# Optimization experiments

Hardware: AMD Instinct MI355X
Metric: run time of the kernel (lower is better)

The kernel has to match this reference:

```python
import jax, jax.numpy as jnp
import numpy as np

N_NODES = 87381  # complete 4-ary tree of depth 9: (4**9 - 1) / 3
VOCAB = 32000
D_IN = 256
M_DIM = 256


def setup_inputs() -> dict:
    key = jax.random.key(0)
    ks = jax.random.split(key, 10)
    w = lambda k, s: jax.random.normal(k, s, dtype=jnp.float32) * 0.05
    return {
        "tokens": jax.random.randint(ks[0], (N_NODES,), 0, VOCAB),
        "branching": 4,
        "emb": w(ks[1], (VOCAB, D_IN)),
        "Wioux": w(ks[2], (D_IN, 3 * M_DIM)),
        "bioux": w(ks[3], (3 * M_DIM,)),
        "Wiouh": w(ks[4], (M_DIM, 3 * M_DIM)),
        "biouh": w(ks[5], (3 * M_DIM,)),
        "Wfx": w(ks[6], (D_IN, M_DIM)),
        "bfx": w(ks[7], (M_DIM,)),
        "Wfh": w(ks[8], (M_DIM, M_DIM)),
        "bfh": w(ks[9], (M_DIM,)),
    }


def _levels(n, b):
    # BFS level boundaries (start, size) for a complete b-ary tree with n nodes
    out, start, size = [], 0, 1
    while start < n:
        out.append((start, min(size, n - start)))
        start += size
        size *= b
    return out


def reference(tokens, branching, emb, Wioux, bioux, Wiouh, biouh, Wfx, bfx, Wfh, bfh):
    N = tokens.shape[0]
    b = int(branching)
    M = Wfh.shape[0]
    x = emb[tokens]                       # [N, D_IN] per-node inputs
    xiou = x @ Wioux + bioux              # [N, 3M] precomputed input gate terms
    xf = x @ Wfx + bfx                    # [N, M]
    h = jnp.zeros((N, M), x.dtype)
    c = jnp.zeros((N, M), x.dtype)
    for (s, sz) in reversed(_levels(N, b)):  # leaves -> root
        idx = jnp.arange(s, s + sz)
        child = idx[:, None] * b + 1 + jnp.arange(b)[None, :]   # [sz, b]
        valid = (child < N)[..., None].astype(x.dtype)          # [sz, b, 1]
        ci = jnp.where(child < N, child, 0)
        ch = h[ci] * valid                                      # [sz, b, M]
        cc = c[ci] * valid
        iou = xiou[idx] + ch.sum(axis=1) @ Wiouh + biouh        # [sz, 3M]
        i, o, u = jnp.split(iou, 3, axis=1)
        i, o, u = jax.nn.sigmoid(i), jax.nn.sigmoid(o), jnp.tanh(u)
        f = jax.nn.sigmoid(ch @ Wfh + bfh + xf[idx][:, None, :])  # [sz, b, M]
        c_new = i * u + jnp.sum(f * cc * valid, axis=1)
        h_new = o * jnp.tanh(c_new)
        c = c.at[idx].set(c_new)
        h = h.at[idx].set(h_new)
    return h  # hidden state of every node; root state is h[0]
```

## Files before the change

kernel.cpp:

```cpp
#include <hip/hip_runtime.h>
#include <cstdint>
#include <cstddef>

typedef _Float16 f16;
typedef __attribute__((ext_vector_type(8))) _Float16 half8;
typedef __attribute__((ext_vector_type(8))) short short8;
typedef __attribute__((ext_vector_type(4))) float floatx4;

#define KDIM 256

__device__ __forceinline__ float sigm(float x) { return 1.0f / (1.0f + __expf(-x)); }

__global__ __launch_bounds__(256) void gemm16(
    const f16* __restrict__ A, const f16* __restrict__ BT,
    f16* __restrict__ C, int ldc_)
{
  __shared__ short lA[64 * 136];
  __shared__ short lB[64 * 136];
  const int t = threadIdx.x;
  const int m0 = blockIdx.x * 64;
  const int n0 = blockIdx.y * 64;
  const int wave = t >> 6;
  const int lane = t & 63;
  const int ln = lane & 15;
  const int quad = lane >> 4;

  floatx4 acc[4];
#pragma unroll
  for (int i = 0; i < 4; ++i) acc[i] = (floatx4){0.f, 0.f, 0.f, 0.f};

#pragma unroll
  for (int kh = 0; kh < 2; ++kh) {
    const int k0 = kh * 128;
#pragma unroll
    for (int i = 0; i < 4; ++i) {
      int chunk = t + 256 * i;
      int row = chunk >> 4;
      int cc = chunk & 15;
      *(short8*)&lA[row * 136 + cc * 8] =
          *(const short8*)(A + (size_t)(m0 + row) * KDIM + k0 + cc * 8);
      *(short8*)&lB[row * 136 + cc * 8] =
          *(const short8*)(BT + (size_t)(n0 + row) * KDIM + k0 + cc * 8);
    }
    __syncthreads();
#pragma unroll
    for (int ks = 0; ks < 4; ++ks) {
      const int kk = ks * 32 + quad * 8;
      half8 a = __builtin_bit_cast(half8,
          *(const short8*)&lA[(wave * 16 + ln) * 136 + kk]);
#pragma unroll
      for (int c = 0; c < 4; ++c) {
        half8 b = __builtin_bit_cast(half8,
            *(const short8*)&lB[(c * 16 + ln) * 136 + kk]);
        acc[c] = __builtin_amdgcn_mfma_f32_16x16x32_f16(a, b, acc[c], 0, 0, 0);
      }
    }
    __syncthreads();
  }
#pragma unroll
  for (int c = 0; c < 4; ++c) {
#pragma unroll
    for (int r = 0; r < 4; ++r) {
      int row = m0 + wave * 16 + quad * 4 + r;
      int col = n0 + c * 16 + ln;
      C[(size_t)row * ldc_ + col] = (f16)acc[c][r];
    }
  }
}

__global__ __launch_bounds__(256) void prep(
    const float* __restrict__ emb, const float* __restrict__ Wioux,
    const float* __restrict__ Wfx, const float* __restrict__ Wiouh,
    const float* __restrict__ Wfh,
    f16* __restrict__ emb_h, f16* __restrict__ BTX,
    f16* __restrict__ WiouhT, f16* __restrict__ WfhT)
{
  int idx = blockIdx.x * 256 + threadIdx.x;
  if (idx < 8192000) {
    emb_h[idx] = (f16)emb[idx];
  } else if (idx < 8454144) {
    int r = idx - 8192000;
    int j = r >> 8, k = r & 255;
    BTX[r] = (f16)((j < 768) ? Wioux[(size_t)k * 768 + j]
                             : Wfx[(size_t)k * 256 + (j - 768)]);
  } else if (idx < 8650752) {
    int r = idx - 8454144;
    int j = r >> 8, k = r & 255;
    WiouhT[r] = (f16)Wiouh[(size_t)k * 768 + j];
  } else {
    int r = idx - 8650752;
    int j = r >> 8, k = r & 255;
    WfhT[r] = (f16)Wfh[(size_t)k * 256 + j];
  }
}

__global__ __launch_bounds__(256) void gather_hsum(
    const float* __restrict__ h, f16* __restrict__ hs, int s)
{
  int r = blockIdx.x;
  int m = threadIdx.x;
  size_t c0 = 4 * (size_t)(s + r) + 1;
  float v = h[c0 * 256 + m] + h[(c0 + 1) * 256 + m] +
            h[(c0 + 2) * 256 + m] + h[(c0 + 3) * 256 + m];
  hs[(size_t)r * 256 + m] = (f16)v;
}

__global__ __launch_bounds__(256) void elem_leaf(
    const int* __restrict__ tokens, const f16* __restrict__ TIOUF,
    const float* __restrict__ bioux, const float* __restrict__ biouh,
    float* __restrict__ cbuf, float* __restrict__ h, f16* __restrict__ h16,
    int s)
{
  int node = s + blockIdx.x;
  int m = threadIdx.x;
  int tok = tokens[node];
  const f16* ti = TIOUF + (size_t)tok * 1024;
  float ip = (float)ti[m]       + bioux[m]       + biouh[m];
  float op = (float)ti[256 + m] + bioux[256 + m] + biouh[256 + m];
  float up = (float)ti[512 + m] + bioux[512 + m] + biouh[512 + m];
  float cv = sigm(ip) * tanhf(up);
  float hv = sigm(op) * tanhf(cv);
  cbuf[(size_t)node * 256 + m] = cv;
  h[(size_t)node * 256 + m] = hv;
  h16[(size_t)node * 256 + m] = (f16)hv;
}

__global__ __launch_bounds__(256) void elem_internal(
    const int* __restrict__ tokens, const f16* __restrict__ TIOUF,
    const f16* __restrict__ IOUH, const f16* __restrict__ FH,
    const float* __restrict__ bioux, const float* __restrict__ biouh,
    const float* __restrict__ bfx, const float* __restrict__ bfh,
    float* __restrict__ cbuf, float* __restrict__ h, f16* __restrict__ h16,
    int s)
{
  int r = blockIdx.x;
  int node = s + r;
  int m = threadIdx.x;
  int tok = tokens[node];
  const f16* ti = TIOUF + (size_t)tok * 1024;
  const f16* io = IOUH + (size_t)r * 768;
  float ip = (float)ti[m]       + (float)io[m]       + bioux[m]       + biouh[m];
  float op = (float)ti[256 + m] + (float)io[256 + m] + bioux[256 + m] + biouh[256 + m];
  float up = (float)ti[512 + m] + (float)io[512 + m] + bioux[512 + m] + biouh[512 + m];
  float xff = (float)ti[768 + m] + bfx[m] + bfh[m];
  float cv = sigm(ip) * tanhf(up);
  size_t child = 4 * (size_t)node + 1;
#pragma unroll
  for (int k = 0; k < 4; ++k) {
    float fk = sigm((float)FH[(child + k) * 256 + m] + xff);
    cv += fk * cbuf[(child + k) * 256 + m];
  }
  float hv = sigm(op) * tanhf(cv);
  cbuf[(size_t)node * 256 + m] = cv;
  h[(size_t)node * 256 + m] = hv;
  h16[(size_t)node * 256 + m] = (f16)hv;
}

extern "C" void kernel_launch(void* const* d_in, const int* in_sizes, int n_in,
                              void* d_out, int out_size, void* d_ws, size_t ws_size,
                              hipStream_t stream) {
  const int*   tokens = (const int*)d_in[0];
  const float* emb    = (const float*)d_in[2];
  const float* Wioux  = (const float*)d_in[3];
  const float* bioux  = (const float*)d_in[4];
  const float* Wiouh  = (const float*)d_in[5];
  const float* biouh  = (const float*)d_in[6];
  const float* Wfx    = (const float*)d_in[7];
  const float* bfx    = (const float*)d_in[8];
  const float* Wfh    = (const float*)d_in[9];
  const float* bfh    = (const float*)d_in[10];
  float* h = (float*)d_out;
  (void)in_sizes; (void)n_in; (void)out_size; (void)ws_size;

  f16* emb_h  = (f16*)d_ws;
  f16* BTX    = emb_h  + 8192000;
  f16* WiouhT = BTX    + 262144;
  f16* WfhT   = WiouhT + 196608;
  f16* TIOUF  = WfhT   + 65536;
  f16* h16    = TIOUF  + (size_t)32768000;
  f16* hs     = h16    + (size_t)22396928;
  f16* IOUH   = hs     + (size_t)4194304;
  f16* FH     = IOUH   + (size_t)12582912;
  float* cbuf = (float*)(FH + (size_t)22396928);

  prep<<<34048, 256, 0, stream>>>(emb, Wioux, Wfx, Wiouh, Wfh,
                                  emb_h, BTX, WiouhT, WfhT);

  gemm16<<<dim3(500, 16), 256, 0, stream>>>(emb_h, BTX, TIOUF, 1024);

  elem_leaf<<<65536, 256, 0, stream>>>(tokens, TIOUF, bioux, biouh,
                                       cbuf, h, h16, 21845);
  gemm16<<<dim3(1024, 4), 256, 0, stream>>>(
      h16 + (size_t)21845 * 256, WfhT, FH + (size_t)21845 * 256, 256);

  const int LS[8][2] = {{5461, 16384}, {1365, 4096}, {341, 1024}, {85, 256},
                        {21, 64},      {5, 16},      {1, 4},      {0, 1}};
  for (int i = 0; i < 8; ++i) {
    int s = LS[i][0], sz = LS[i][1];
    int mt = (sz + 63) / 64;
    gather_hsum<<<sz, 256, 0, stream>>>(h, hs, s);
    gemm16<<<dim3(mt, 12), 256, 0, stream>>>(hs, WiouhT, IOUH, 768);
    elem_internal<<<sz, 256, 0, stream>>>(tokens, TIOUF, IOUH, FH,
                                          bioux, biouh, bfx, bfh,
                                          cbuf, h, h16, s);
    if (s > 0)
      gemm16<<<dim3(mt, 4), 256, 0, stream>>>(
          h16 + (size_t)s * 256, WfhT, FH + (size_t)s * 256, 256);
  }
}
```

Measured before the change: 434.8 us.

## Fuse per-level elementwise update, parent child-sum and forget-gate GEMM into one kernel

Replaces the separate gather_hsum, elem_leaf/elem_internal and per-level Wfh GEMM launches with a single level_fused kernel. Each block handles 64 consecutive nodes: it computes their cell and hidden states and stages fp16 h in shared memory. From there it sums sibling groups into the parent-level hsum buffer and runs the h·Wfh MFMA GEMM in-block to produce FH. This removes the h16 round trip through global memory and about half the launches per level. In exchange, each block walks its 64 nodes serially in the elementwise phase, so far fewer blocks run per level, which can expose memory latency.

After: 853.3 us. +96.3%, slower.

```diff
diff --git a/kernel.cpp b/kernel.cpp
--- a/kernel.cpp
+++ b/kernel.cpp
@@ -94,66 +94,120 @@
   }
 }
 
-__global__ __launch_bounds__(256) void gather_hsum(
-    const float* __restrict__ h, f16* __restrict__ hs, int s)
-{
-  int r = blockIdx.x;
-  int m = threadIdx.x;
-  size_t c0 = 4 * (size_t)(s + r) + 1;
-  float v = h[c0 * 256 + m] + h[(c0 + 1) * 256 + m] +
-            h[(c0 + 2) * 256 + m] + h[(c0 + 3) * 256 + m];
-  hs[(size_t)r * 256 + m] = (f16)v;
-}
-
-__global__ __launch_bounds__(256) void elem_leaf(
+__global__ __launch_bounds__(256) void level_fused(
     const int* __restrict__ tokens, const f16* __restrict__ TIOUF,
-    const float* __restrict__ bioux, const float* __restrict__ biouh,
-    float* __restrict__ cbuf, float* __restrict__ h, f16* __restrict__ h16,
-    int s)
-{
-  int node = s + blockIdx.x;
-  int m = threadIdx.x;
-  int tok = tokens[node];
-  const f16* ti = TIOUF + (size_t)tok * 1024;
-  float ip = (float)ti[m]       + bioux[m]       + biouh[m];
-  float op = (float)ti[256 + m] + bioux[256 + m] + biouh[256 + m];
-  float up = (float)ti[512 + m] + bioux[512 + m] + biouh[512 + m];
-  float cv = sigm(ip) * tanhf(up);
-  float hv = sigm(op) * tanhf(cv);
-  cbuf[(size_t)node * 256 + m] = cv;
-  h[(size_t)node * 256 + m] = hv;
-  h16[(size_t)node * 256 + m] = (f16)hv;
-}
-
-__global__ __launch_bounds__(256) void elem_internal(
-    const int* __restrict__ tokens, const f16* __restrict__ TIOUF,
-    const f16* __restrict__ IOUH, const f16* __restrict__ FH,
+    const f16* __restrict__ IOUH, f16* FH,
+    const f16* __restrict__ WfhT,
     const float* __restrict__ bioux, const float* __restrict__ biouh,
     const float* __restrict__ bfx, const float* __restrict__ bfh,
-    float* __restrict__ cbuf, float* __restrict__ h, f16* __restrict__ h16,
-    int s)
+    float* cbuf, float* __restrict__ h, f16* __restrict__ hsum16,
+    int s, int sz, int s_up, int sz_up, int leaf)
 {
-  int r = blockIdx.x;
-  int node = s + r;
-  int m = threadIdx.x;
-  int tok = tokens[node];
-  const f16* ti = TIOUF + (size_t)tok * 1024;
-  const f16* io = IOUH + (size_t)r * 768;
-  float ip = (float)ti[m]       + (float)io[m]       + bioux[m]       + biouh[m];
-  float op = (float)ti[256 + m] + (float)io[256 + m] + bioux[256 + m] + biouh[256 + m];
-  float up = (float)ti[512 + m] + (float)io[512 + m] + bioux[512 + m] + biouh[512 + m];
-  float xff = (float)ti[768 + m] + bfx[m] + bfh[m];
-  float cv = sigm(ip) * tanhf(up);
-  size_t child = 4 * (size_t)node + 1;
-#pragma unroll
-  for (int k = 0; k < 4; ++k) {
-    float fk = sigm((float)FH[(child + k) * 256 + m] + xff);
-    cv += fk * cbuf[(child + k) * 256 + m];
-  }
-  float hv = sigm(op) * tanhf(cv);
-  cbuf[(size_t)node * 256 + m] = cv;
-  h[(size_t)node * 256 + m] = hv;
-  h16[(size_t)node * 256 + m] = (f16)hv;
+  __shared__ f16 hA[64 * 264];
+  __shared__ f16 lB[64 * 264];
+  __shared__ int ltok[64];
+
+  const int t = threadIdx.x;
+  const int base = s + 64 * blockIdx.x;
+  const int lim = s + sz;
+
+  if (t < 64) ltok[t] = (base + t < lim) ? tokens[base + t] : 0;
+  __syncthreads();
+
+  const int m = t;
+  const float bi0 = bioux[m] + biouh[m];
+  const float bi1 = bioux[256 + m] + biouh[256 + m];
+  const float bi2 = bioux[512 + m] + biouh[512 + m];
+  const float bf = bfx[m] + bfh[m];
+  for (int n = 0; n < 64; ++n) {
+    int node = base + n;
+    if (node < lim) {
+      const f16* ti = TIOUF + (size_t)ltok[n] * 1024;
+      float ip = (float)ti[m] + bi0;
+      float op = (float)ti[256 + m] + bi1;
+      float up = (float)ti[512 + m] + bi2;
+      float cv;
+      if (leaf) {
+        cv = sigm(ip) * tanhf(up);
+      } else {
+        const f16* io = IOUH + (size_t)(node - s) * 768;
+        ip += (float)io[m];
+        op += (float)io[256 + m];
+        up += (float)io[512 + m];
+        float xff = (float)ti[768 + m] + bf;
+        cv = sigm(ip) * tanhf(up);
+        size_t ch = 4 * (size_t)node + 1;
+#pragma unroll
+        for (int k = 0; k < 4; ++k) {
+          float fk = sigm((float)FH[(ch + k) * 256 + m] + xff);
+          cv += fk * cbuf[(ch + k) * 256 + m];
+        }
+      }
+      float hv = sigm(op) * tanhf(cv);
+      cbuf[(size_t)node * 256 + m] = cv;
+      h[(size_t)node * 256 + m] = hv;
+      hA[n * 264 + m] = (f16)hv;
+    } else {
+      hA[n * 264 + m] = (f16)0.f;
+    }
+  }
+  __syncthreads();
+
+  if (s_up >= 0) {
+    int P0 = (base - 1) >> 2;
+#pragma unroll
+    for (int p = 0; p < 16; ++p) {
+      if (P0 + p < s_up + sz_up) {
+        float v = (float)hA[(4 * p + 0) * 264 + m] + (float)hA[(4 * p + 1) * 264 + m] +
+                  (float)hA[(4 * p + 2) * 264 + m] + (float)hA[(4 * p + 3) * 264 + m];
+        hsum16[(size_t)(P0 + p - s_up) * 256 + m] = (f16)v;
+      }
+    }
+  }
+
+  if (s != 0) {
+    const int wave = t >> 6;
+    const int lane = t & 63;
+    const int ln = lane & 15;
+    const int quad = lane >> 4;
+    for (int nc = 0; nc < 4; ++nc) {
+      const int n0 = nc * 64;
+#pragma unroll
+      for (int i = 0; i < 8; ++i) {
+        int chunk = t + 256 * i;
+        int row = chunk >> 5;
+        int cc = chunk & 31;
+        *(short8*)&lB[row * 264 + cc * 8] =
+            *(const short8*)(WfhT + (size_t)(n0 + row) * 256 + cc * 8);
+      }
+      __syncthreads();
+      floatx4 acc[4];
+#pragma unroll
+      for (int i = 0; i < 4; ++i) acc[i] = (floatx4){0.f, 0.f, 0.f, 0.f};
+#pragma unroll
+      for (int ks = 0; ks < 8; ++ks) {
+        const int kk = ks * 32 + quad * 8;
+        half8 a = __builtin_bit_cast(half8,
+            *(const short8*)&hA[(wave * 16 + ln) * 264 + kk]);
+#pragma unroll
+        for (int c = 0; c < 4; ++c) {
+          half8 b = __builtin_bit_cast(half8,
+              *(const short8*)&lB[(c * 16 + ln) * 264 + kk]);
+          acc[c] = __builtin_amdgcn_mfma_f32_16x16x32_f16(a, b, acc[c], 0, 0, 0);
+        }
+      }
+#pragma unroll
+      for (int c = 0; c < 4; ++c) {
+#pragma unroll
+        for (int r = 0; r < 4; ++r) {
+          int row = wave * 16 + quad * 4 + r;
+          int col = n0 + c * 16 + ln;
+          FH[((size_t)(base + row)) * 256 + col] = (f16)acc[c][r];
+        }
+      }
+      __syncthreads();
+    }
+  }
 }
 
 extern "C" void kernel_launch(void* const* d_in, const int* in_sizes, int n_in,
@@ -172,39 +226,35 @@
   float* h = (float*)d_out;
   (void)in_sizes; (void)n_in; (void)out_size; (void)ws_size;
 
-  f16* emb_h  = (f16*)d_ws;
-  f16* BTX    = emb_h  + 8192000;
-  f16* WiouhT = BTX    + 262144;
-  f16* WfhT   = WiouhT + 196608;
-  f16* TIOUF  = WfhT   + 65536;
-  f16* h16    = TIOUF  + (size_t)32768000;
-  f16* hs     = h16    + (size_t)22396928;
-  f16* IOUH   = hs     + (size_t)4194304;
-  f16* FH     = IOUH   + (size_t)12582912;
-  float* cbuf = (float*)(FH + (size_t)22396928);
+  f16* emb_h   = (f16*)d_ws;
+  f16* BTX     = emb_h   + 8192000;
+  f16* WiouhT  = BTX     + 262144;
+  f16* WfhT    = WiouhT  + 196608;
+  f16* TIOUF   = WfhT    + 65536;
+  f16* IOUH    = TIOUF   + (size_t)32768000;
+  f16* FH      = IOUH    + (size_t)12582912;
+  f16* hsum16  = FH      + (size_t)22396928;
+  float* cbuf  = (float*)(hsum16 + (size_t)4194304);
 
   prep<<<34048, 256, 0, stream>>>(emb, Wioux, Wfx, Wiouh, Wfh,
                                   emb_h, BTX, WiouhT, WfhT);
 
   gemm16<<<dim3(500, 16), 256, 0, stream>>>(emb_h, BTX, TIOUF, 1024);
 
-  elem_leaf<<<65536, 256, 0, stream>>>(tokens, TIOUF, bioux, biouh,
-                                       cbuf, h, h16, 21845);
-  gemm16<<<dim3(1024, 4), 256, 0, stream>>>(
-      h16 + (size_t)21845 * 256, WfhT, FH + (size_t)21845 * 256, 256);
-
-  const int LS[8][2] = {{5461, 16384}, {1365, 4096}, {341, 1024}, {85, 256},
-                        {21, 64},      {5, 16},      {1, 4},      {0, 1}};
+  level_fused<<<1024, 256, 0, stream>>>(tokens, TIOUF, nullptr, FH, WfhT,
+                                        bioux, biouh, bfx, bfh, cbuf, h, hsum16,
+                                        21845, 65536, 5461, 16384, 1);
+
+  const int LS[8][4] = {{5461, 16384, 1365, 4096}, {1365, 4096, 341, 1024},
+                        {341, 1024, 85, 256},      {85, 256, 21, 64},
+                        {21, 64, 5, 16},           {5, 16, 1, 4},
+                        {1, 4, 0, 1},              {0, 1, -1, 0}};
   for (int i = 0; i < 8; ++i) {
-    int s = LS[i][0], sz = LS[i][1];
+    int s = LS[i][0], sz = LS[i][1], s_up = LS[i][2], sz_up = LS[i][3];
     int mt = (sz + 63) / 64;
-    gather_hsum<<<sz, 256, 0, stream>>>(h, hs, s);
-    gemm16<<<dim3(mt, 12), 256, 0, stream>>>(hs, WiouhT, IOUH, 768);
-    elem_internal<<<sz, 256, 0, stream>>>(tokens, TIOUF, IOUH, FH,
-                                          bioux, biouh, bfx, bfh,
-                                          cbuf, h, h16, s);
-    if (s > 0)
-      gemm16<<<dim3(mt, 4), 256, 0, stream>>>(
-          h16 + (size_t)s * 256, WfhT, FH + (size_t)s * 256, 256);
-  }
-}
+    gemm16<<<dim3(mt, 12), 256, 0, stream>>>(hsum16, WiouhT, IOUH, 768);
+    level_fused<<<mt, 256, 0, stream>>>(tokens, TIOUF, IOUH, FH, WfhT,
+                                        bioux, biouh, bfx, bfh, cbuf, h, hsum16,
+                                        s, sz, s_up, sz_up, 0);
+  }
+}
```
